# Optimization experiments

Measured on AMD Instinct MI355X. Metric: run time of the kernel, lower is better.

Reference implementation:

```python
import jax, jax.numpy as jnp
import numpy as np
import math

HIDDEN = 1024
HEADS = 8
HEAD = HIDDEN // HEADS
B, S = 2, 2048
SCALE_BASE = 512
EPS = 1e-5


def _xpos(x, downscale=False):
    # x: [..., S, d]  (canonical RetNet XPOS: rotate_every_two + xpos scaling)
    d = x.shape[-1]
    s = x.shape[-2]
    half = d // 2
    scale_vec = (jnp.arange(0, d, 2, dtype=jnp.float32) + 0.4 * d) / (1.4 * d)  # [half]
    pos = jnp.arange(s, dtype=jnp.float32)
    scale = scale_vec[None, :] ** (pos[:, None] / SCALE_BASE)                    # [S, half]
    inv_freq = 1.0 / (10000.0 ** (jnp.arange(half, dtype=jnp.float32) / half))
    ang = pos[:, None] * inv_freq[None, :]                                       # [S, half]
    sin, cos = jnp.sin(ang), jnp.cos(ang)
    if downscale:
        scale = 1.0 / scale
    sinp = jnp.repeat(sin * scale, 2, axis=-1)  # duplicate_interleave -> [S, d]
    cosp = jnp.repeat(cos * scale, 2, axis=-1)
    x1, x2 = x[..., ::2], x[..., 1::2]
    rot = jnp.stack([-x2, x1], axis=-1).reshape(x.shape)  # rotate_every_two
    return x * cosp + rot * sinp


def _gammas(h):
    return 1.0 - jnp.exp(jnp.linspace(math.log(1.0 / 32), math.log(1.0 / 512), h)).astype(jnp.float32)


def setup_inputs() -> dict:
    key = jax.random.key(0)
    ks = jax.random.split(key, 6)
    X = jax.random.normal(ks[0], (B, S, HIDDEN), dtype=jnp.float32)
    W_Q = jax.random.normal(ks[1], (HEADS, HIDDEN, HEAD), dtype=jnp.float32) / HIDDEN
    W_K = jax.random.normal(ks[2], (HEADS, HIDDEN, HEAD), dtype=jnp.float32) / HIDDEN
    W_V = jax.random.normal(ks[3], (HEADS, HIDDEN, HEAD), dtype=jnp.float32) / HIDDEN
    W_G = jax.random.normal(ks[4], (HIDDEN, HIDDEN), dtype=jnp.float32) / HIDDEN
    W_O = jax.random.normal(ks[5], (HIDDEN, HIDDEN), dtype=jnp.float32) / HIDDEN
    gn_weight = jnp.ones((HIDDEN,), dtype=jnp.float32)
    gn_bias = jnp.zeros((HIDDEN,), dtype=jnp.float32)
    return dict(X=X, W_Q=W_Q, W_K=W_K, W_V=W_V, W_G=W_G, W_O=W_O,
                gn_weight=gn_weight, gn_bias=gn_bias)


def reference(X, W_Q, W_K, W_V, W_G, W_O, gn_weight, gn_bias):
    b, s, _ = X.shape
    h, _, dv = W_V.shape
    Q = _xpos(jnp.einsum('bse,hed->bhsd', X, W_Q))
    K = _xpos(jnp.einsum('bse,hed->bhsd', X, W_K), downscale=True)
    V = jnp.einsum('bse,hed->bhsd', X, W_V)
    gam = _gammas(h)
    n = jnp.arange(s)
    diff = n[:, None] - n[None, :]
    mask = diff >= 0
    # per-head causal decay mask D[h, n, m] = gamma_h**(n-m) for n>=m else 0
    D = jnp.where(mask[None],
                  gam[:, None, None] ** jnp.where(mask, diff, 0)[None].astype(jnp.float32),
                  0.0)                                             # [H,S,S]
    scores = jnp.einsum('bhsd,bhtd->bhst', Q, K) * D[None]         # [B,H,S,S]
    Y = jnp.einsum('bhst,bhtv->bhsv', scores, V)                   # [B,H,S,dv]
    Y = jnp.transpose(Y, (0, 2, 1, 3))                             # [B,S,H,dv] (head concat)
    # GroupNorm(heads, v_dim) over flattened (B*S, v_dim): normalize within each head group
    mu = Y.mean(-1, keepdims=True)
    var = Y.var(-1, keepdims=True)
    Yn = ((Y - mu) / jnp.sqrt(var + EPS)).reshape(b, s, h * dv) * gn_weight + gn_bias
    gate = X @ W_G
    gate = gate * jax.nn.sigmoid(gate)  # swish
    return (gate * Yn) @ W_O
```

## Files before the change

### kernel.cpp

```cpp
#include <hip/hip_runtime.h>
#include <hip/hip_bf16.h>
#include <math.h>

namespace {

constexpr int Bc = 2;
constexpr int Sc = 2048;
constexpr int Ec = 1024;
constexpr int Hc = 8;
constexpr int Dc = 128;
constexpr int Mc = Bc * Sc;

typedef unsigned short u16;
typedef u16    u16x8  __attribute__((ext_vector_type(8)));
typedef u16    u16x4  __attribute__((ext_vector_type(4)));
typedef __bf16 bf16x8 __attribute__((ext_vector_type(8)));
typedef float  f32x4  __attribute__((ext_vector_type(4)));

static __device__ inline bf16x8 asbf(u16x8 v) { return __builtin_bit_cast(bf16x8, v); }

static __device__ inline f32x4 mfma16(u16x8 a, u16x8 b, f32x4 c) {
    return __builtin_amdgcn_mfma_f32_16x16x32_bf16(asbf(a), asbf(b), c, 0, 0, 0);
}

static __device__ inline u16 f2bf(float f) {
    unsigned u = __builtin_bit_cast(unsigned, f);
    return (u16)((u + 0x7fffu + ((u >> 16) & 1u)) >> 16);
}
static __device__ inline float bf2f(u16 h) {
    unsigned u = ((unsigned)h) << 16;
    return __builtin_bit_cast(float, u);
}

static __device__ inline void gload16(const u16* g, u16* l) {
    __builtin_amdgcn_global_load_lds(
        (__attribute__((address_space(1))) void*)const_cast<u16*>(g),
        (__attribute__((address_space(3))) void*)l,
        16, 0, 0);
}

__global__ __launch_bounds__(256) void convX(const float* __restrict__ in,
                                             u16* __restrict__ out, int n8)
{
    int i = blockIdx.x * 256 + threadIdx.x;
    if (i >= n8) return;
    float4 a = *(const float4*)(in + (size_t)i * 8);
    float4 b = *(const float4*)(in + (size_t)i * 8 + 4);
    u16x8 o;
    o[0] = f2bf(a.x); o[1] = f2bf(a.y); o[2] = f2bf(a.z); o[3] = f2bf(a.w);
    o[4] = f2bf(b.x); o[5] = f2bf(b.y); o[6] = f2bf(b.z); o[7] = f2bf(b.w);
    *(u16x8*)(out + (size_t)i * 8) = o;
}

__global__ __launch_bounds__(256) void tconvH(const float* __restrict__ p0,
                                              const float* __restrict__ p1,
                                              const float* __restrict__ p2,
                                              u16* __restrict__ out)
{
    const int z = blockIdx.z;
    const float* ip = (z < 8 ? p0 : z < 16 ? p1 : p2) + (size_t)(z & 7) * Ec * Dc;
    u16* op = out + (size_t)z * Dc * Ec;
    __shared__ float tile[32][33];
    const int r0 = blockIdx.x * 32, c0 = blockIdx.y * 32;
    const int ty = threadIdx.x >> 5, tx = threadIdx.x & 31;
#pragma unroll
    for (int i = ty; i < 32; i += 8) tile[i][tx] = ip[(size_t)(r0 + i) * Dc + c0 + tx];
    __syncthreads();
#pragma unroll
    for (int i = ty; i < 32; i += 8) op[(size_t)(c0 + i) * Ec + r0 + tx] = f2bf(tile[tx][i]);
}

__global__ __launch_bounds__(256) void tconvSq(const float* __restrict__ p0,
                                               const float* __restrict__ p1,
                                               u16* __restrict__ out)
{
    const int z = blockIdx.z;
    const float* ip = z == 0 ? p0 : p1;
    u16* op = out + (size_t)z * Ec * Ec;
    __shared__ float tile[32][33];
    const int r0 = blockIdx.x * 32, c0 = blockIdx.y * 32;
    const int ty = threadIdx.x >> 5, tx = threadIdx.x & 31;
#pragma unroll
    for (int i = ty; i < 32; i += 8) tile[i][tx] = ip[(size_t)(r0 + i) * Ec + c0 + tx];
    __syncthreads();
#pragma unroll
    for (int i = ty; i < 32; i += 8) op[(size_t)(c0 + i) * Ec + r0 + tx] = f2bf(tile[tx][i]);
}

__global__ __launch_bounds__(256) void trigk(float2* __restrict__ tabQ,
                                             float2* __restrict__ tabK)
{
    int t = blockIdx.x * 256 + threadIdx.x;
    int s = t >> 6, ip = t & 63;
    float sv = (2.f * (float)ip + 51.2f) * (1.f / 179.2f);
    float sc = exp2f(((float)s * (1.f / 512.f)) * log2f(sv));
    float freq = exp2f(-(float)ip * (13.287712379549449f / 64.f));
    float ang = (float)s * freq;
    float sn, cs;
    sincosf(ang, &sn, &cs);
    tabQ[t] = make_float2(cs * sc, sn * sc);
    tabK[t] = make_float2(cs / sc, sn / sc);
}

__global__ __launch_bounds__(512, 2) void mgemm4(const u16* __restrict__ A,
                                                 const u16* __restrict__ Ball,
                                                 u16* __restrict__ Qo,
                                                 u16* __restrict__ Ko,
                                                 u16* __restrict__ Vo,
                                                 u16* __restrict__ Go,
                                                 const float2* __restrict__ tabQ,
                                                 const float2* __restrict__ tabK)
{
    const int t = threadIdx.x, lane = t & 63, wid = t >> 6;
    const int wm = wid >> 2, wn = wid & 3;
    const int rl = lane & 15, hi = lane >> 4;
    const int r0 = blockIdx.x * 256;
    const int wsel = blockIdx.y >> 2;
    const int n0 = (blockIdx.y & 3) * 256;
    const u16* Bt = Ball + (size_t)wsel * Ec * Ec;

    __shared__ u16 lds[2][2][256 * 64];

    f32x4 acc[8][4] = {};

    const int srow = lane >> 3;
    const int scol = (((lane & 7) ^ srow) << 3);
    const u16* Asrc = A  + (size_t)(r0 + wid * 32 + srow) * Ec + scol;
    const u16* Bsrc = Bt + (size_t)(n0 + wid * 32 + srow) * Ec + scol;

#define STAGE256(tile, buf)                                                     \
    do {                                                                        \
        const int _k0 = (tile) * 64;                                            \
        _Pragma("unroll")                                                       \
        for (int i = 0; i < 4; ++i) {                                           \
            gload16(Asrc + (size_t)(i * 8) * Ec + _k0,                          \
                    &lds[buf][0][(wid * 32 + i * 8) * 64]);                     \
            gload16(Bsrc + (size_t)(i * 8) * Ec + _k0,                          \
                    &lds[buf][1][(wid * 32 + i * 8) * 64]);                     \
        }                                                                       \
    } while (0)

    STAGE256(0, 0);
    for (int tt = 0; tt < 16; ++tt) {
        const int buf = tt & 1;
        if (tt + 1 < 16) {
            STAGE256(tt + 1, buf ^ 1);
            asm volatile("s_waitcnt vmcnt(8)" ::: "memory");
        } else {
            asm volatile("s_waitcnt vmcnt(0)" ::: "memory");
        }
        __builtin_amdgcn_s_barrier();

        u16x8 breg[4][2];
#pragma unroll
        for (int cf = 0; cf < 4; ++cf)
#pragma unroll
            for (int ks = 0; ks < 2; ++ks) {
                const int row = wn * 64 + cf * 16 + rl;
                breg[cf][ks] = *(const u16x8*)
                    &lds[buf][1][row * 64 + ((ks * 32 + hi * 8) ^ ((rl & 7) << 3))];
            }
#pragma unroll
        for (int q = 0; q < 4; ++q) {
            u16x8 areg[2][2];
#pragma unroll
            for (int rfi = 0; rfi < 2; ++rfi)
#pragma unroll
                for (int ks = 0; ks < 2; ++ks) {
                    const int row = wm * 128 + (q * 2 + rfi) * 16 + rl;
                    areg[rfi][ks] = *(const u16x8*)
                        &lds[buf][0][row * 64 + ((ks * 32 + hi * 8) ^ ((rl & 7) << 3))];
                }
            __builtin_amdgcn_s_setprio(1);
#pragma unroll
            for (int rfi = 0; rfi < 2; ++rfi)
#pragma unroll
                for (int cf = 0; cf < 4; ++cf)
#pragma unroll
                    for (int ks = 0; ks < 2; ++ks)
                        acc[q * 2 + rfi][cf] =
                            mfma16(breg[cf][ks], areg[rfi][ks], acc[q * 2 + rfi][cf]);
            __builtin_amdgcn_s_setprio(0);
        }
        __builtin_amdgcn_s_barrier();
    }
#undef STAGE256

    u16* Cout = wsel == 0 ? Qo : wsel == 1 ? Ko : wsel == 2 ? Vo : Go;
    const float2* tab = wsel == 0 ? tabQ : tabK;

#pragma unroll
    for (int rf = 0; rf < 8; ++rf) {
        const int row = r0 + wm * 128 + rf * 16 + rl;
#pragma unroll
        for (int cf = 0; cf < 4; ++cf) {
            const int col0 = n0 + wn * 64 + cf * 16 + hi * 4;
            f32x4 v = acc[rf][cf];
            if (wsel <= 1) {
                const size_t tb = (size_t)(row & 2047) * 64 + ((col0 >> 1) & 63);
                const float2 c0 = tab[tb];
                const float2 c1 = tab[tb + 1];
                float e0 = v[0], o0 = v[1], e1 = v[2], o1 = v[3];
                v[0] = e0 * c0.x - o0 * c0.y;
                v[1] = o0 * c0.x + e0 * c0.y;
                v[2] = e1 * c1.x - o1 * c1.y;
                v[3] = o1 * c1.x + e1 * c1.y;
            } else if (wsel == 3) {
#pragma unroll
                for (int r = 0; r < 4; ++r) v[r] = v[r] / (1.f + expf(-v[r]));
            }
            u16x4 pk;
#pragma unroll
            for (int r = 0; r < 4; ++r) pk[r] = f2bf(v[r]);
            *(u16x4*)(Cout + (size_t)row * Ec + col0) = pk;
        }
    }
}

#define GCORE_STAGE(lA, lB, k0)                                   \
    do {                                                          \
        gload16(Ag + (k0),                  (lA) + w * 1024);     \
        gload16(Ag + 16 * Ec + (k0),        (lA) + w * 1024 + 512);\
        gload16(Bg + (k0),                  (lB) + w * 1024);     \
        gload16(Bg + 16 * Ec + (k0),        (lB) + w * 1024 + 512);\
    } while (0)

#define GCORE_COMPUTE(lA, lB)                                                 \
    do {                                                                      \
        u16x8 bfr[8];                                                         \
        _Pragma("unroll")                                                     \
        for (int ct = 0; ct < 8; ++ct)                                        \
            bfr[ct] = *(const u16x8*)&(lB)[(ct * 16 + rl) * 32 + hi * 8];     \
        _Pragma("unroll")                                                     \
        for (int rt = 0; rt < 2; ++rt) {                                      \
            u16x8 afr = *(const u16x8*)&(lA)[(w * 32 + rt * 16 + rl) * 32 + hi * 8]; \
            _Pragma("unroll")                                                 \
            for (int ct = 0; ct < 8; ++ct)                                    \
                acc[rt][ct] = mfma16(bfr[ct], afr, acc[rt][ct]);              \
        }                                                                     \
    } while (0)

#define GCORE_SYNC()                                              \
    do {                                                          \
        asm volatile("s_waitcnt vmcnt(0)" ::: "memory");          \
        __builtin_amdgcn_s_barrier();                             \
    } while (0)

__global__ __launch_bounds__(256) void mgemmO(const u16* __restrict__ A,
                                              const u16* __restrict__ Bt,
                                              float* __restrict__ Cout)
{
    const int t = threadIdx.x;
    const int lane = t & 63, w = t >> 6;
    const int rl = lane & 15, hi = lane >> 4;
    const int r0 = blockIdx.x * 128;
    const int n0 = blockIdx.y * 128;

    __shared__ u16 As0[4096], As1[4096], Bs0[4096], Bs1[4096];

    f32x4 acc[2][8] = {};

    const u16* Ag = A  + (size_t)(r0 + w * 32 + (lane >> 2)) * Ec + (lane & 3) * 8;
    const u16* Bg = Bt + (size_t)(n0 + w * 32 + (lane >> 2)) * Ec + (lane & 3) * 8;

    GCORE_STAGE(As0, Bs0, 0);
    GCORE_SYNC();
    for (int k0 = 0; k0 < Ec; k0 += 64) {
        GCORE_STAGE(As1, Bs1, k0 + 32);
        GCORE_COMPUTE(As0, Bs0);
        GCORE_SYNC();
        if (k0 + 64 < Ec) GCORE_STAGE(As0, Bs0, k0 + 64);
        GCORE_COMPUTE(As1, Bs1);
        GCORE_SYNC();
    }

#pragma unroll
    for (int rt = 0; rt < 2; ++rt) {
        const int row = r0 + w * 32 + rt * 16 + rl;
#pragma unroll
        for (int ct = 0; ct < 8; ++ct) {
            const int col0 = n0 + ct * 16 + hi * 4;
            *(f32x4*)(Cout + (size_t)row * Ec + col0) = acc[rt][ct];
        }
    }
}

__global__ __launch_bounds__(256) void ret_gn(const u16* __restrict__ Q,
                                              const u16* __restrict__ K,
                                              const u16* __restrict__ V,
                                              const u16* __restrict__ G,
                                              const float* __restrict__ gw,
                                              const float* __restrict__ gbias,
                                              u16* __restrict__ Z)
{
    const int t = threadIdx.x, lane = t & 63, w = t >> 6;
    const int rl = lane & 15, hi = lane >> 4;
    const int id = blockIdx.x;
    const int slot = id & 15;
    const int a  = id >> 4;
    const int rb = (a < 16) ? (31 - a) : (a - 16);
    const int b = slot >> 3;
    const int h = b == 0 ? (slot & 7) : 7 - (slot & 7);

    __shared__ u16 Ks[2][64][136];
    __shared__ u16 Vt[2][128][68];
    __shared__ u16 Ss[64][72];

    const float lga = -3.4657359027997265f;
    const float lgb = -6.2383246250395075f;
    const float gamma = 1.f - expf(lga + (float)h * (lgb - lga) * (1.f / 7.f));
    const float lg2 = log2f(gamma);

    int c_lo = 0;
    {
        float cut = 9.2103404f / (-logf(gamma));
        int mmin = rb * 64 - (int)cut;
        if (mmin > 0) c_lo = mmin >> 6;
    }

    const int ki = t >> 2,        kq = (t & 3) * 32;
    const int vm4 = (t & 15) * 4, vd = (t >> 4) * 8;
    const u16* Kg0 = K + (size_t)(b * Sc) * Ec + h * Dc;
    const u16* Vg0 = V + (size_t)(b * Sc) * Ec + h * Dc;

    u16x8 kreg[4], vreg[4];
    {
        const u16* Kg = Kg0 + (size_t)(c_lo * 64 + ki) * Ec + kq;
#pragma unroll
        for (int r = 0; r < 4; ++r) kreg[r] = *(const u16x8*)(Kg + r * 8);
        const u16* Vg = Vg0 + (size_t)(c_lo * 64 + vm4) * Ec + vd;
#pragma unroll
        for (int r = 0; r < 4; ++r) vreg[r] = *(const u16x8*)(Vg + (size_t)r * Ec);
    }

    {
        const int i = t >> 2, q = (t & 3) * 32;
        const u16* Qg = Q + (size_t)(b * Sc + rb * 64 + i) * Ec + h * Dc + q;
        u16x8 v0 = *(const u16x8*)(Qg);
        u16x8 v1 = *(const u16x8*)(Qg + 8);
        u16x8 v2 = *(const u16x8*)(Qg + 16);
        u16x8 v3 = *(const u16x8*)(Qg + 24);
        *(u16x8*)&Ks[0][i][q]      = v0;
        *(u16x8*)&Ks[0][i][q + 8]  = v1;
        *(u16x8*)&Ks[0][i][q + 16] = v2;
        *(u16x8*)&Ks[0][i][q + 24] = v3;
    }
    __syncthreads();
    u16x8 qf[4][4];
#pragma unroll
    for (int nt = 0; nt < 4; ++nt)
#pragma unroll
        for (int ks = 0; ks < 4; ++ks)
            qf[nt][ks] = *(const u16x8*)&Ks[0][nt * 16 + rl][ks * 32 + hi * 8];
    __syncthreads();

    float mf[4];
#pragma unroll
    for (int reg = 0; reg < 4; ++reg)
        mf[reg] = exp2f(-lg2 * (float)(w * 16 + hi * 4 + reg));
    float nf[4];
#pragma unroll
    for (int nt = 0; nt < 4; ++nt)
        nf[nt] = exp2f(lg2 * (float)((rb - c_lo) * 64 + nt * 16 + rl));
    const float ginv64 = exp2f(-lg2 * 64.f);

    f32x4 yacc[8] = {};

    for (int c = c_lo; c <= rb; ++c) {
        const int cur = c & 1;
#pragma unroll
        for (int r = 0; r < 4; ++r)
            *(u16x8*)&Ks[cur][ki][kq + r * 8] = kreg[r];
#pragma unroll
        for (int j = 0; j < 8; ++j) {
            u16x4 p;
            p[0] = vreg[0][j]; p[1] = vreg[1][j]; p[2] = vreg[2][j]; p[3] = vreg[3][j];
            *(u16x4*)&Vt[cur][vd + j][vm4] = p;
        }
        __syncthreads();
        if (c < rb) {
            const u16* Kg = Kg0 + (size_t)((c + 1) * 64 + ki) * Ec + kq;
#pragma unroll
            for (int r = 0; r < 4; ++r) kreg[r] = *(const u16x8*)(Kg + r * 8);
            const u16* Vg = Vg0 + (size_t)((c + 1) * 64 + vm4) * Ec + vd;
#pragma unroll
            for (int r = 0; r < 4; ++r) vreg[r] = *(const u16x8*)(Vg + (size_t)r * Ec);
        }

        __builtin_amdgcn_s_setprio(1);
        u16x8 kf[4];
#pragma unroll
        for (int ks = 0; ks < 4; ++ks)
            kf[ks] = *(const u16x8*)&Ks[cur][w * 16 + rl][ks * 32 + hi * 8];
#pragma unroll
        for (int nt = 0; nt < 4; ++nt) {
            f32x4 s = {};
#pragma unroll
            for (int ks = 0; ks < 4; ++ks)
                s = mfma16(kf[ks], qf[nt][ks], s);
            u16x4 pk;
#pragma unroll
            for (int reg = 0; reg < 4; ++reg) {
                float wgt = nf[nt] * mf[reg];
                if (c == rb && (w * 16 + hi * 4 + reg) > (nt * 16 + rl)) wgt = 0.f;
                pk[reg] = f2bf(s[reg] * wgt);
            }
            *(u16x4*)&Ss[nt * 16 + rl][w * 16 + hi * 4] = pk;
        }
        __builtin_amdgcn_s_setprio(0);
        __syncthreads();

        u16x8 sf0 = *(const u16x8*)&Ss[w * 16 + rl][hi * 8];
        u16x8 sf1 = *(const u16x8*)&Ss[w * 16 + rl][32 + hi * 8];
        __builtin_amdgcn_s_setprio(1);
#pragma unroll
        for (int ct = 0; ct < 8; ++ct) {
            u16x8 vf0 = *(const u16x8*)&Vt[cur][ct * 16 + rl][hi * 8];
            u16x8 vf1 = *(const u16x8*)&Vt[cur][ct * 16 + rl][32 + hi * 8];
            yacc[ct] = mfma16(vf0, sf0, yacc[ct]);
            yacc[ct] = mfma16(vf1, sf1, yacc[ct]);
        }
        __builtin_amdgcn_s_setprio(0);
#pragma unroll
        for (int nt = 0; nt < 4; ++nt) nf[nt] *= ginv64;
    }

    const int nloc = w * 16 + rl;
    const size_t row = (size_t)(b * Sc + rb * 64 + nloc);
    float s = 0.f, sq = 0.f;
#pragma unroll
    for (int ct = 0; ct < 8; ++ct)
#pragma unroll
        for (int reg = 0; reg < 4; ++reg) {
            float v = yacc[ct][reg];
            s += v; sq += v * v;
        }
    s  += __shfl_xor(s, 16);  sq += __shfl_xor(sq, 16);
    s  += __shfl_xor(s, 32);  sq += __shfl_xor(sq, 32);
    const float mu  = s * (1.f / 128.f);
    const float var = sq * (1.f / 128.f) - mu * mu;
    const float inv = rsqrtf(var + 1e-5f);
#pragma unroll
    for (int ct = 0; ct < 8; ++ct) {
        const int col0 = h * Dc + ct * 16 + hi * 4;
        const f32x4 w4 = *(const f32x4*)(gw + col0);
        const f32x4 b4 = *(const f32x4*)(gbias + col0);
        const u16x4 g4 = *(const u16x4*)(G + row * Ec + col0);
        u16x4 z4;
#pragma unroll
        for (int reg = 0; reg < 4; ++reg)
            z4[reg] = f2bf(((yacc[ct][reg] - mu) * inv * w4[reg] + b4[reg]) * bf2f(g4[reg]));
        *(u16x4*)(Z + row * Ec + col0) = z4;
    }
}

}

extern "C" void kernel_launch(void* const* d_in, const int* in_sizes, int n_in,
                              void* d_out, int out_size, void* d_ws, size_t ws_size,
                              hipStream_t stream)
{
    const float* X    = (const float*)d_in[0];
    const float* W_Q  = (const float*)d_in[1];
    const float* W_K  = (const float*)d_in[2];
    const float* W_V  = (const float*)d_in[3];
    const float* W_G  = (const float*)d_in[4];
    const float* W_O  = (const float*)d_in[5];
    const float* gw   = (const float*)d_in[6];
    const float* gb   = (const float*)d_in[7];

    char* ws = (char*)d_ws;
    const size_t NX = (size_t)Mc * Ec;
    u16*    Xb   = (u16*)ws;                ws += NX * 2;
    u16*    WqT  = (u16*)ws;                ws += (size_t)Ec * Ec * 2;
    u16*    WkT  = (u16*)ws;                ws += (size_t)Ec * Ec * 2;
    u16*    WvT  = (u16*)ws;                ws += (size_t)Ec * Ec * 2;
    u16*    WgT  = (u16*)ws;                ws += (size_t)Ec * Ec * 2;
    u16*    WoT  = (u16*)ws;                ws += (size_t)Ec * Ec * 2;
    float2* tabQ = (float2*)ws;             ws += (size_t)Sc * 64 * sizeof(float2);
    float2* tabK = (float2*)ws;             ws += (size_t)Sc * 64 * sizeof(float2);
    u16*    Qb   = (u16*)ws;                ws += NX * 2;
    u16*    Kb   = (u16*)ws;                ws += NX * 2;
    u16*    Vb   = (u16*)ws;                ws += NX * 2;
    u16*    Gb   = (u16*)ws;                ws += NX * 2;
    u16*    Zb   = (u16*)ws;                ws += NX * 2;
    (void)WkT; (void)WvT; (void)WgT;

    dim3 blk(256);
    convX<<<dim3((int)(NX / 8 / 256)), blk, 0, stream>>>(X, Xb, (int)(NX / 8));
    tconvH<<<dim3(32, 4, 24), blk, 0, stream>>>(W_Q, W_K, W_V, WqT);
    tconvSq<<<dim3(32, 32, 2), blk, 0, stream>>>(W_G, W_O, WgT);
    trigk<<<dim3(Sc * 64 / 256), blk, 0, stream>>>(tabQ, tabK);

    mgemm4<<<dim3(Mc / 256, 16), dim3(512), 0, stream>>>(Xb, WqT, Qb, Kb, Vb, Gb, tabQ, tabK);

    ret_gn<<<dim3(512), blk, 0, stream>>>(Qb, Kb, Vb, Gb, gw, gb, Zb);

    mgemmO<<<dim3(Mc / 128, Ec / 128), blk, 0, stream>>>(Zb, WoT, (float*)d_out);
}
```

Baseline: 134.1 us.

## Fuse prep kernels, shrink GEMM K-tiles for occupancy, narrow output GEMM tiles

Four preprocessing kernels (X conversion, weight transposes, trig table) are merged into a single launch to cut launch overhead. The fused QKVG GEMM drops its K-tile from 64 to 32, halving LDS use so the launch bound can go from 2 to 4 blocks per CU, and switches to a new XOR swizzle. The output GEMM moves to 128x64 tiles with double-buffered 32-wide K stages and the same swizzle, giving more blocks. The trade is more barriers per K and less MFMA work between synchronisations.

```diff
diff --git a/kernel.cpp b/kernel.cpp
--- a/kernel.cpp
+++ b/kernel.cpp
@@ -39,70 +39,70 @@
         16, 0, 0);
 }
 
-__global__ __launch_bounds__(256) void convX(const float* __restrict__ in,
-                                             u16* __restrict__ out, int n8)
+#define AIDX(R_, hi_) (((R_) * 32) + (((hi_) ^ (((R_) >> 1) & 3)) << 3))
+
+__global__ __launch_bounds__(256) void prep(const float* __restrict__ X,
+                                            const float* __restrict__ W_Q,
+                                            const float* __restrict__ W_K,
+                                            const float* __restrict__ W_V,
+                                            const float* __restrict__ W_G,
+                                            const float* __restrict__ W_O,
+                                            u16* __restrict__ Xb,
+                                            u16* __restrict__ Wh,
+                                            u16* __restrict__ Wsq,
+                                            float2* __restrict__ tabQ,
+                                            float2* __restrict__ tabK)
 {
-    int i = blockIdx.x * 256 + threadIdx.x;
-    if (i >= n8) return;
-    float4 a = *(const float4*)(in + (size_t)i * 8);
-    float4 b = *(const float4*)(in + (size_t)i * 8 + 4);
-    u16x8 o;
-    o[0] = f2bf(a.x); o[1] = f2bf(a.y); o[2] = f2bf(a.z); o[3] = f2bf(a.w);
-    o[4] = f2bf(b.x); o[5] = f2bf(b.y); o[6] = f2bf(b.z); o[7] = f2bf(b.w);
-    *(u16x8*)(out + (size_t)i * 8) = o;
-}
-
-__global__ __launch_bounds__(256) void tconvH(const float* __restrict__ p0,
-                                              const float* __restrict__ p1,
-                                              const float* __restrict__ p2,
-                                              u16* __restrict__ out)
-{
-    const int z = blockIdx.z;
-    const float* ip = (z < 8 ? p0 : z < 16 ? p1 : p2) + (size_t)(z & 7) * Ec * Dc;
-    u16* op = out + (size_t)z * Dc * Ec;
+    const int bid = blockIdx.x, tid = threadIdx.x;
     __shared__ float tile[32][33];
-    const int r0 = blockIdx.x * 32, c0 = blockIdx.y * 32;
-    const int ty = threadIdx.x >> 5, tx = threadIdx.x & 31;
-#pragma unroll
-    for (int i = ty; i < 32; i += 8) tile[i][tx] = ip[(size_t)(r0 + i) * Dc + c0 + tx];
-    __syncthreads();
-#pragma unroll
-    for (int i = ty; i < 32; i += 8) op[(size_t)(c0 + i) * Ec + r0 + tx] = f2bf(tile[tx][i]);
-}
-
-__global__ __launch_bounds__(256) void tconvSq(const float* __restrict__ p0,
-                                               const float* __restrict__ p1,
-                                               u16* __restrict__ out)
-{
-    const int z = blockIdx.z;
-    const float* ip = z == 0 ? p0 : p1;
-    u16* op = out + (size_t)z * Ec * Ec;
-    __shared__ float tile[32][33];
-    const int r0 = blockIdx.x * 32, c0 = blockIdx.y * 32;
-    const int ty = threadIdx.x >> 5, tx = threadIdx.x & 31;
-#pragma unroll
-    for (int i = ty; i < 32; i += 8) tile[i][tx] = ip[(size_t)(r0 + i) * Ec + c0 + tx];
-    __syncthreads();
-#pragma unroll
-    for (int i = ty; i < 32; i += 8) op[(size_t)(c0 + i) * Ec + r0 + tx] = f2bf(tile[tx][i]);
-}
-
-__global__ __launch_bounds__(256) void trigk(float2* __restrict__ tabQ,
-                                             float2* __restrict__ tabK)
-{
-    int t = blockIdx.x * 256 + threadIdx.x;
-    int s = t >> 6, ip = t & 63;
-    float sv = (2.f * (float)ip + 51.2f) * (1.f / 179.2f);
-    float sc = exp2f(((float)s * (1.f / 512.f)) * log2f(sv));
-    float freq = exp2f(-(float)ip * (13.287712379549449f / 64.f));
-    float ang = (float)s * freq;
-    float sn, cs;
-    sincosf(ang, &sn, &cs);
-    tabQ[t] = make_float2(cs * sc, sn * sc);
-    tabK[t] = make_float2(cs / sc, sn / sc);
-}
-
-__global__ __launch_bounds__(512, 2) void mgemm4(const u16* __restrict__ A,
+
+    if (bid < 2048) {
+        const int i = bid * 256 + tid;
+        float4 a = *(const float4*)(X + (size_t)i * 8);
+        float4 b = *(const float4*)(X + (size_t)i * 8 + 4);
+        u16x8 o;
+        o[0] = f2bf(a.x); o[1] = f2bf(a.y); o[2] = f2bf(a.z); o[3] = f2bf(a.w);
+        o[4] = f2bf(b.x); o[5] = f2bf(b.y); o[6] = f2bf(b.z); o[7] = f2bf(b.w);
+        *(u16x8*)(Xb + (size_t)i * 8) = o;
+    } else if (bid < 5120) {
+        const int idx = bid - 2048;
+        const int z = idx >> 7, rem = idx & 127;
+        const int r0 = (rem >> 2) * 32, c0 = (rem & 3) * 32;
+        const float* ip = (z < 8 ? W_Q : z < 16 ? W_K : W_V) + (size_t)(z & 7) * Ec * Dc;
+        u16* op = Wh + (size_t)z * Dc * Ec;
+        const int ty = tid >> 5, tx = tid & 31;
+#pragma unroll
+        for (int i = ty; i < 32; i += 8) tile[i][tx] = ip[(size_t)(r0 + i) * Dc + c0 + tx];
+        __syncthreads();
+#pragma unroll
+        for (int i = ty; i < 32; i += 8) op[(size_t)(c0 + i) * Ec + r0 + tx] = f2bf(tile[tx][i]);
+    } else if (bid < 7168) {
+        const int idx = bid - 5120;
+        const int z = idx >> 10, rem = idx & 1023;
+        const int r0 = (rem >> 5) * 32, c0 = (rem & 31) * 32;
+        const float* ip = z == 0 ? W_G : W_O;
+        u16* op = Wsq + (size_t)z * Ec * Ec;
+        const int ty = tid >> 5, tx = tid & 31;
+#pragma unroll
+        for (int i = ty; i < 32; i += 8) tile[i][tx] = ip[(size_t)(r0 + i) * Ec + c0 + tx];
+        __syncthreads();
+#pragma unroll
+        for (int i = ty; i < 32; i += 8) op[(size_t)(c0 + i) * Ec + r0 + tx] = f2bf(tile[tx][i]);
+    } else {
+        const int i = (bid - 7168) * 256 + tid;
+        const int s = i >> 6, ip = i & 63;
+        float sv = (2.f * (float)ip + 51.2f) * (1.f / 179.2f);
+        float sc = exp2f(((float)s * (1.f / 512.f)) * log2f(sv));
+        float freq = exp2f(-(float)ip * (13.287712379549449f / 64.f));
+        float ang = (float)s * freq;
+        float sn, cs;
+        sincosf(ang, &sn, &cs);
+        tabQ[i] = make_float2(cs * sc, sn * sc);
+        tabK[i] = make_float2(cs / sc, sn / sc);
+    }
+}
+
+__global__ __launch_bounds__(512, 4) void mgemm4(const u16* __restrict__ A,
                                                  const u16* __restrict__ Ball,
                                                  u16* __restrict__ Qo,
                                                  u16* __restrict__ Ko,
@@ -119,72 +119,58 @@
     const int n0 = (blockIdx.y & 3) * 256;
     const u16* Bt = Ball + (size_t)wsel * Ec * Ec;
 
-    __shared__ u16 lds[2][2][256 * 64];
+    __shared__ u16 lds[2][2][256 * 32];
 
     f32x4 acc[8][4] = {};
 
-    const int srow = lane >> 3;
-    const int scol = (((lane & 7) ^ srow) << 3);
-    const u16* Asrc = A  + (size_t)(r0 + wid * 32 + srow) * Ec + scol;
-    const u16* Bsrc = Bt + (size_t)(n0 + wid * 32 + srow) * Ec + scol;
-
-#define STAGE256(tile, buf)                                                     \
+    const int srow = lane >> 2;
+    const int schunk = (lane & 3) ^ ((lane >> 3) & 3);
+    const u16* Asrc = A  + (size_t)(r0 + wid * 32 + srow) * Ec + schunk * 8;
+    const u16* Bsrc = Bt + (size_t)(n0 + wid * 32 + srow) * Ec + schunk * 8;
+
+#define STAGE32(tile_, buf_)                                                    \
     do {                                                                        \
-        const int _k0 = (tile) * 64;                                            \
-        _Pragma("unroll")                                                       \
-        for (int i = 0; i < 4; ++i) {                                           \
-            gload16(Asrc + (size_t)(i * 8) * Ec + _k0,                          \
-                    &lds[buf][0][(wid * 32 + i * 8) * 64]);                     \
-            gload16(Bsrc + (size_t)(i * 8) * Ec + _k0,                          \
-                    &lds[buf][1][(wid * 32 + i * 8) * 64]);                     \
-        }                                                                       \
+        const int _k0 = (tile_) * 32;                                           \
+        gload16(Asrc + _k0,                     &lds[buf_][0][(wid * 32) * 32]);      \
+        gload16(Asrc + (size_t)16 * Ec + _k0,   &lds[buf_][0][(wid * 32 + 16) * 32]); \
+        gload16(Bsrc + _k0,                     &lds[buf_][1][(wid * 32) * 32]);      \
+        gload16(Bsrc + (size_t)16 * Ec + _k0,   &lds[buf_][1][(wid * 32 + 16) * 32]); \
     } while (0)
 
-    STAGE256(0, 0);
-    for (int tt = 0; tt < 16; ++tt) {
+    STAGE32(0, 0);
+    for (int tt = 0; tt < 32; ++tt) {
         const int buf = tt & 1;
-        if (tt + 1 < 16) {
-            STAGE256(tt + 1, buf ^ 1);
-            asm volatile("s_waitcnt vmcnt(8)" ::: "memory");
+        if (tt + 1 < 32) {
+            STAGE32(tt + 1, buf ^ 1);
+            asm volatile("s_waitcnt vmcnt(4)" ::: "memory");
         } else {
             asm volatile("s_waitcnt vmcnt(0)" ::: "memory");
         }
         __builtin_amdgcn_s_barrier();
 
-        u16x8 breg[4][2];
+        u16x8 breg[4];
 #pragma unroll
         for (int cf = 0; cf < 4; ++cf)
-#pragma unroll
-            for (int ks = 0; ks < 2; ++ks) {
-                const int row = wn * 64 + cf * 16 + rl;
-                breg[cf][ks] = *(const u16x8*)
-                    &lds[buf][1][row * 64 + ((ks * 32 + hi * 8) ^ ((rl & 7) << 3))];
-            }
+            breg[cf] = *(const u16x8*)&lds[buf][1][AIDX(wn * 64 + cf * 16 + rl, hi)];
 #pragma unroll
         for (int q = 0; q < 4; ++q) {
-            u16x8 areg[2][2];
+            u16x8 areg[2];
 #pragma unroll
             for (int rfi = 0; rfi < 2; ++rfi)
-#pragma unroll
-                for (int ks = 0; ks < 2; ++ks) {
-                    const int row = wm * 128 + (q * 2 + rfi) * 16 + rl;
-                    areg[rfi][ks] = *(const u16x8*)
-                        &lds[buf][0][row * 64 + ((ks * 32 + hi * 8) ^ ((rl & 7) << 3))];
-                }
+                areg[rfi] = *(const u16x8*)
+                    &lds[buf][0][AIDX(wm * 128 + (q * 2 + rfi) * 16 + rl, hi)];
             __builtin_amdgcn_s_setprio(1);
 #pragma unroll
             for (int rfi = 0; rfi < 2; ++rfi)
 #pragma unroll
                 for (int cf = 0; cf < 4; ++cf)
-#pragma unroll
-                    for (int ks = 0; ks < 2; ++ks)
-                        acc[q * 2 + rfi][cf] =
-                            mfma16(breg[cf][ks], areg[rfi][ks], acc[q * 2 + rfi][cf]);
+                    acc[q * 2 + rfi][cf] =
+                        mfma16(breg[cf], areg[rfi], acc[q * 2 + rfi][cf]);
             __builtin_amdgcn_s_setprio(0);
         }
         __builtin_amdgcn_s_barrier();
     }
-#undef STAGE256
+#undef STAGE32
 
     u16* Cout = wsel == 0 ? Qo : wsel == 1 ? Ko : wsel == 2 ? Vo : Go;
     const float2* tab = wsel == 0 ? tabQ : tabK;
@@ -217,70 +203,69 @@
     }
 }
 
-#define GCORE_STAGE(lA, lB, k0)                                   \
-    do {                                                          \
-        gload16(Ag + (k0),                  (lA) + w * 1024);     \
-        gload16(Ag + 16 * Ec + (k0),        (lA) + w * 1024 + 512);\
-        gload16(Bg + (k0),                  (lB) + w * 1024);     \
-        gload16(Bg + 16 * Ec + (k0),        (lB) + w * 1024 + 512);\
-    } while (0)
-
-#define GCORE_COMPUTE(lA, lB)                                                 \
-    do {                                                                      \
-        u16x8 bfr[8];                                                         \
-        _Pragma("unroll")                                                     \
-        for (int ct = 0; ct < 8; ++ct)                                        \
-            bfr[ct] = *(const u16x8*)&(lB)[(ct * 16 + rl) * 32 + hi * 8];     \
-        _Pragma("unroll")                                                     \
-        for (int rt = 0; rt < 2; ++rt) {                                      \
-            u16x8 afr = *(const u16x8*)&(lA)[(w * 32 + rt * 16 + rl) * 32 + hi * 8]; \
-            _Pragma("unroll")                                                 \
-            for (int ct = 0; ct < 8; ++ct)                                    \
-                acc[rt][ct] = mfma16(bfr[ct], afr, acc[rt][ct]);              \
-        }                                                                     \
-    } while (0)
-
-#define GCORE_SYNC()                                              \
-    do {                                                          \
-        asm volatile("s_waitcnt vmcnt(0)" ::: "memory");          \
-        __builtin_amdgcn_s_barrier();                             \
-    } while (0)
-
 __global__ __launch_bounds__(256) void mgemmO(const u16* __restrict__ A,
                                               const u16* __restrict__ Bt,
                                               float* __restrict__ Cout)
 {
-    const int t = threadIdx.x;
-    const int lane = t & 63, w = t >> 6;
+    const int t = threadIdx.x, lane = t & 63, w = t >> 6;
     const int rl = lane & 15, hi = lane >> 4;
     const int r0 = blockIdx.x * 128;
-    const int n0 = blockIdx.y * 128;
-
-    __shared__ u16 As0[4096], As1[4096], Bs0[4096], Bs1[4096];
-
-    f32x4 acc[2][8] = {};
-
-    const u16* Ag = A  + (size_t)(r0 + w * 32 + (lane >> 2)) * Ec + (lane & 3) * 8;
-    const u16* Bg = Bt + (size_t)(n0 + w * 32 + (lane >> 2)) * Ec + (lane & 3) * 8;
-
-    GCORE_STAGE(As0, Bs0, 0);
-    GCORE_SYNC();
-    for (int k0 = 0; k0 < Ec; k0 += 64) {
-        GCORE_STAGE(As1, Bs1, k0 + 32);
-        GCORE_COMPUTE(As0, Bs0);
-        GCORE_SYNC();
-        if (k0 + 64 < Ec) GCORE_STAGE(As0, Bs0, k0 + 64);
-        GCORE_COMPUTE(As1, Bs1);
-        GCORE_SYNC();
-    }
-
-#pragma unroll
-    for (int rt = 0; rt < 2; ++rt) {
-        const int row = r0 + w * 32 + rt * 16 + rl;
-#pragma unroll
-        for (int ct = 0; ct < 8; ++ct) {
-            const int col0 = n0 + ct * 16 + hi * 4;
-            *(f32x4*)(Cout + (size_t)row * Ec + col0) = acc[rt][ct];
+    const int n0 = blockIdx.y * 64;
+
+    __shared__ u16 Ab[2][128 * 32];
+    __shared__ u16 Bb[2][64 * 32];
+
+    f32x4 acc[2][4] = {};
+
+    const int srow = lane >> 2;
+    const int schunk = (lane & 3) ^ ((lane >> 3) & 3);
+    const u16* Asrc = A  + (size_t)(r0 + w * 32 + srow) * Ec + schunk * 8;
+    const u16* Bsrc = Bt + (size_t)(n0 + w * 16 + srow) * Ec + schunk * 8;
+
+#define STAGEO(tile_, buf_)                                                   \
+    do {                                                                      \
+        const int _k0 = (tile_) * 32;                                         \
+        gload16(Asrc + _k0,                   &Ab[buf_][(w * 32) * 32]);      \
+        gload16(Asrc + (size_t)16 * Ec + _k0, &Ab[buf_][(w * 32 + 16) * 32]); \
+        gload16(Bsrc + _k0,                   &Bb[buf_][(w * 16) * 32]);      \
+    } while (0)
+
+    STAGEO(0, 0);
+    for (int tt = 0; tt < 32; ++tt) {
+        const int buf = tt & 1;
+        if (tt + 1 < 32) {
+            STAGEO(tt + 1, buf ^ 1);
+            asm volatile("s_waitcnt vmcnt(3)" ::: "memory");
+        } else {
+            asm volatile("s_waitcnt vmcnt(0)" ::: "memory");
+        }
+        __builtin_amdgcn_s_barrier();
+
+        u16x8 breg[4], areg[2];
+#pragma unroll
+        for (int cf = 0; cf < 4; ++cf)
+            breg[cf] = *(const u16x8*)&Bb[buf][AIDX(cf * 16 + rl, hi)];
+#pragma unroll
+        for (int rfi = 0; rfi < 2; ++rfi)
+            areg[rfi] = *(const u16x8*)&Ab[buf][AIDX(w * 32 + rfi * 16 + rl, hi)];
+        __builtin_amdgcn_s_setprio(1);
+#pragma unroll
+        for (int rfi = 0; rfi < 2; ++rfi)
+#pragma unroll
+            for (int cf = 0; cf < 4; ++cf)
+                acc[rfi][cf] = mfma16(breg[cf], areg[rfi], acc[rfi][cf]);
+        __builtin_amdgcn_s_setprio(0);
+        __builtin_amdgcn_s_barrier();
+    }
+#undef STAGEO
+
+#pragma unroll
+    for (int rfi = 0; rfi < 2; ++rfi) {
+        const int row = r0 + w * 32 + rfi * 16 + rl;
+#pragma unroll
+        for (int cf = 0; cf < 4; ++cf) {
+            const int col0 = n0 + cf * 16 + hi * 4;
+            *(f32x4*)(Cout + (size_t)row * Ec + col0) = acc[rfi][cf];
         }
     }
 }
@@ -484,17 +469,14 @@
     u16*    Vb   = (u16*)ws;                ws += NX * 2;
     u16*    Gb   = (u16*)ws;                ws += NX * 2;
     u16*    Zb   = (u16*)ws;                ws += NX * 2;
-    (void)WkT; (void)WvT; (void)WgT;
-
-    dim3 blk(256);
-    convX<<<dim3((int)(NX / 8 / 256)), blk, 0, stream>>>(X, Xb, (int)(NX / 8));
-    tconvH<<<dim3(32, 4, 24), blk, 0, stream>>>(W_Q, W_K, W_V, WqT);
-    tconvSq<<<dim3(32, 32, 2), blk, 0, stream>>>(W_G, W_O, WgT);
-    trigk<<<dim3(Sc * 64 / 256), blk, 0, stream>>>(tabQ, tabK);
+    (void)WkT; (void)WvT;
+
+    prep<<<dim3(7680), dim3(256), 0, stream>>>(X, W_Q, W_K, W_V, W_G, W_O,
+                                               Xb, WqT, WgT, tabQ, tabK);
 
     mgemm4<<<dim3(Mc / 256, 16), dim3(512), 0, stream>>>(Xb, WqT, Qb, Kb, Vb, Gb, tabQ, tabK);
 
-    ret_gn<<<dim3(512), blk, 0, stream>>>(Qb, Kb, Vb, Gb, gw, gb, Zb);
-
-    mgemmO<<<dim3(Mc / 128, Ec / 128), blk, 0, stream>>>(Zb, WoT, (float*)d_out);
-}
+    ret_gn<<<dim3(512), dim3(256), 0, stream>>>(Qb, Kb, Vb, Gb, gw, gb, Zb);
+
+    mgemmO<<<dim3(Mc / 128, Ec / 64), dim3(256), 0, stream>>>(Zb, WoT, (float*)d_out);
+}
```

Result: slower. 253.7 us (+89.2%).
